# Kernel optimization log

Measured on AMD Instinct MI355X. Metric: run time of the kernel, lower is better.

Reference implementation:

```python
import jax, jax.numpy as jnp
import numpy as np

KERNEL = 3
STRIDE = 1
PADDING = 1


def _extract_patches(x, k, stride, padding, h_out, w_out):
    # x: [B, C, H, W] -> patches [k, k, B, C, h_out, w_out]
    if padding > 0:
        x = jnp.pad(x, ((0, 0), (0, 0), (padding, padding), (padding, padding)))
    rows = []
    for di in range(k):
        cols = []
        for dj in range(k):
            sl = x[:, :, di:di + (h_out - 1) * stride + 1:stride,
                        dj:dj + (w_out - 1) * stride + 1:stride]
            cols.append(sl)
        rows.append(jnp.stack(cols, axis=0))
    return jnp.stack(rows, axis=0)  # [k, k, B, C, h_out, w_out]


def setup_inputs() -> dict:
    key = jax.random.key(0)
    k1, k2 = jax.random.split(key)
    B, C_in, C_out, H, W = 32, 64, 64, 32, 32
    h_out = (H + 2 * PADDING - KERNEL) // STRIDE + 1
    w_out = (W + 2 * PADDING - KERNEL) // STRIDE + 1
    fan_in = C_in * KERNEL ** 2
    x = jax.random.normal(k1, (B, C_in, H, W), dtype=jnp.float32)
    weight = jax.random.normal(
        k2, (h_out, w_out, C_out, C_in, KERNEL, KERNEL), dtype=jnp.float32
    ) / np.sqrt(fan_in).astype(np.float32)
    bias = jnp.zeros((C_out, h_out, w_out), dtype=jnp.float32)
    return {"x": x, "weight": weight, "bias": bias}


def reference(x, weight, bias):
    h_out, w_out = weight.shape[0], weight.shape[1]
    # patches: [k, k, B, C, h_out, w_out]
    patches = _extract_patches(x, KERNEL, STRIDE, PADDING, h_out, w_out)
    # unshared-weight contraction per spatial location
    # weight: [h_out(x), w_out(y), O, C(i), k(k), k(l)]
    out = jnp.einsum('xyoikl,klbixy->boxy', weight, patches)
    return out + bias[None, :, :, :]
```

## Files before the change

kernel.cpp:

```cpp
#include <hip/hip_runtime.h>

#define HH 32
#define WW 32
#define CIN 64
#define COUT 64
#define BATCH 32
#define KTOT 576
#define NPOS 1024
#define KC 16
#define KHALF 288
#define NCW 18
#define WGRP 260

__device__ float g_xT[CIN * 34 * 34 * BATCH];

__global__ __launch_bounds__(256) void repack_kernel(const float* __restrict__ x) {
    __shared__ float tile[32 * 33];
    const int i   = blockIdx.x;
    const int hh  = blockIdx.y;
    const int tid = threadIdx.x;

    float* dst = &g_xT[((i * 34 + hh) * 34) * BATCH];

    if (hh == 0 || hh == 33) {
        for (int idx = tid; idx < 34 * BATCH; idx += 256) dst[idx] = 0.f;
        return;
    }
    const int hs = hh - 1;
#pragma unroll
    for (int bb = 0; bb < 4; ++bb) {
        int b = bb * 8 + (tid >> 5);
        int w = tid & 31;
        tile[b * 33 + w] = x[(b << 16) + (i << 10) + (hs << 5) + w];
    }
    __syncthreads();
#pragma unroll
    for (int q = 0; q < 5; ++q) {
        int ww = q * 8 + (tid >> 5);
        if (ww < 34) {
            int b = tid & 31;
            float v = (ww == 0 || ww == 33) ? 0.f : tile[b * 33 + (ww - 1)];
            dst[ww * BATCH + b] = v;
        }
    }
}

__device__ __forceinline__ void async16(const void* src, void* dst_lds) {
    __builtin_amdgcn_global_load_lds(
        (const __attribute__((address_space(1))) void*)src,
        (__attribute__((address_space(3))) void*)dst_lds,
        16, 0, 0);
}

__global__ __launch_bounds__(128, 2) void local2d_kernel(
    const float* __restrict__ weight,
    const float* __restrict__ bias,
    float* __restrict__ out)
{
    __shared__ float Wl[2][3][4 * WGRP];
    __shared__ float Pl[2][3][KC * BATCH];

    const int wv = threadIdx.x >> 6;
    const int l  = threadIdx.x & 63;

    const int og = l & 7, bg = l >> 3;

    int bid = blockIdx.x;
    int xcd = bid & 7;
    int t   = bid >> 3;
    int y   = ((t >> 5) << 3) | xcd;
    int xw  = t & 31;
    int p   = (y << 5) | xw;

    const int kbase = wv * KHALF;
    const float* wpos  = weight + (long)p * (COUT * KTOT);
    const float* wsrc0 = wpos + (l >> 2) * KTOT + ((l & 3) << 2) + kbase;

    float acc[8][4];
#pragma unroll
    for (int a = 0; a < 8; ++a)
#pragma unroll
        for (int c = 0; c < 4; ++c) acc[a][c] = 0.f;

    auto stage = [&](int c, int bsel) {
        const float* ws = wsrc0 + c * KC;
#pragma unroll
        for (int g = 0; g < 4; ++g)
            async16(ws + g * (16 * KTOT), &Wl[wv][bsel][g * WGRP]);
#pragma unroll
        for (int q = 0; q < 2; ++q) {
            int k  = kbase + c * KC + (q << 3) + (l >> 3);
            int i  = k / 9;
            int r  = k - i * 9;
            int kh = r / 3;
            int kw = r - kh * 3;
            const float* ps =
                &g_xT[(((i * 34) + y + kh) * 34 + xw + kw) * BATCH + ((l & 7) << 2)];
            async16(ps, &Pl[wv][bsel][q * (8 * BATCH)]);
        }
    };

    auto compute = [&](int bsel) {
        const float* Wb = &Wl[wv][bsel][(og >> 1) * WGRP + ((og & 1) << 3) * 16];
        const float* Pb = &Pl[wv][bsel][bg << 2];
#pragma unroll
        for (int kk = 0; kk < KC; kk += 4) {
            float4 pr[4];
#pragma unroll
            for (int j = 0; j < 4; ++j)
                pr[j] = *(const float4*)(Pb + (kk + j) * BATCH);
            const float* prf = (const float*)pr;
#pragma unroll
            for (int oo = 0; oo < 8; ++oo) {
                float4 wr = *(const float4*)(Wb + oo * KC + kk);
#pragma unroll
                for (int bb = 0; bb < 4; ++bb) {
                    float a = acc[oo][bb];
                    a = fmaf(wr.x, prf[0 * 4 + bb], a);
                    a = fmaf(wr.y, prf[1 * 4 + bb], a);
                    a = fmaf(wr.z, prf[2 * 4 + bb], a);
                    a = fmaf(wr.w, prf[3 * 4 + bb], a);
                    acc[oo][bb] = a;
                }
            }
        }
    };

    stage(0, 0);
    stage(1, 1);
    for (int c = 0; c < NCW - 1; ++c) {
        asm volatile("s_waitcnt vmcnt(6)" ::: "memory");
        asm volatile("s_waitcnt lgkmcnt(0)" ::: "memory");
        if (c + 2 < NCW) stage(c + 2, (c + 2) % 3);
        compute(c % 3);
    }
    asm volatile("s_waitcnt vmcnt(0)" ::: "memory");
    compute((NCW - 1) % 3);

    __syncthreads();
    float* R = &Wl[1][0][0];
    if (wv == 1) {
#pragma unroll
        for (int oo = 0; oo < 8; ++oo) {
            int o = (og << 3) + oo;
            *(float4*)(&R[o * 36 + (bg << 2)]) =
                make_float4(acc[oo][0], acc[oo][1], acc[oo][2], acc[oo][3]);
        }
    }
    __syncthreads();
    if (wv == 0) {
#pragma unroll
        for (int oo = 0; oo < 8; ++oo) {
            int o = (og << 3) + oo;
            float bv = bias[(o << 10) + p];
            float4 r = *(const float4*)(&R[o * 36 + (bg << 2)]);
            const float* rf = (const float*)&r;
#pragma unroll
            for (int bb = 0; bb < 4; ++bb) {
                int b = (bg << 2) + bb;
                out[(b << 16) + (o << 10) + p] = acc[oo][bb] + rf[bb] + bv;
            }
        }
    }
}

extern "C" void kernel_launch(void* const* d_in, const int* in_sizes, int n_in,
                              void* d_out, int out_size, void* d_ws, size_t ws_size,
                              hipStream_t stream) {
    const float* x      = (const float*)d_in[0];
    const float* weight = (const float*)d_in[1];
    const float* bias   = (const float*)d_in[2];
    float* out          = (float*)d_out;

    hipLaunchKernelGGL(repack_kernel, dim3(CIN, 34), dim3(256), 0, stream, x);
    hipLaunchKernelGGL(local2d_kernel, dim3(NPOS), dim3(128), 0, stream,
                       weight, bias, out);
}
```

Baseline: 243.1 us.

## Split output channels across two blocks per position with double-buffered LDS staging

Each spatial position is now handled by two blocks, one for each half of the output channels. This doubles the grid and cuts per-thread accumulators from 32 to 16, and launch bounds are raised to allow 4 blocks per SIMD for more occupancy. The weight LDS layout is transposed so that o is contiguous per k, and the pipeline moves from triple to double buffering, issuing the next stage after compute. In exchange, each block loads its patch data twice, since both halves need the full patch.

```diff
diff --git a/kernel.cpp b/kernel.cpp
--- a/kernel.cpp
+++ b/kernel.cpp
@@ -10,7 +10,6 @@
 #define KC 16
 #define KHALF 288
 #define NCW 18
-#define WGRP 260
 
 __device__ float g_xT[CIN * 34 * 34 * BATCH];
 
@@ -52,13 +51,12 @@
         16, 0, 0);
 }
 
-__global__ __launch_bounds__(128, 2) void local2d_kernel(
+__global__ __launch_bounds__(128, 4) void local2d_kernel(
     const float* __restrict__ weight,
     const float* __restrict__ bias,
     float* __restrict__ out)
 {
-    __shared__ float Wl[2][3][4 * WGRP];
-    __shared__ float Pl[2][3][KC * BATCH];
+    __shared__ __align__(16) float lds[4096];
 
     const int wv = threadIdx.x >> 6;
     const int l  = threadIdx.x & 63;
@@ -68,25 +66,33 @@
     int bid = blockIdx.x;
     int xcd = bid & 7;
     int t   = bid >> 3;
-    int y   = ((t >> 5) << 3) | xcd;
-    int xw  = t & 31;
+    int oh  = t & 1;
+    int tt  = t >> 1;
+    int y   = ((tt >> 5) << 3) | xcd;
+    int xw  = tt & 31;
     int p   = (y << 5) | xw;
 
     const int kbase = wv * KHALF;
-    const float* wpos  = weight + (long)p * (COUT * KTOT);
-    const float* wsrc0 = wpos + (l >> 2) * KTOT + ((l & 3) << 2) + kbase;
+    const float* wpos = weight + ((long)p * COUT + (oh << 5)) * KTOT;
 
-    float acc[8][4];
+    const int rem = l & 31;
+    const int wo  = ((rem & 7) << 2) + (rem >> 3);
+    const float* wsrc0 = wpos + wo * KTOT + kbase + ((l >> 5) << 2);
+
+    float* Wb = &lds[wv << 10];
+    float* Pb = &lds[2048 + (wv << 10)];
+
+    float acc[4][4];
 #pragma unroll
-    for (int a = 0; a < 8; ++a)
+    for (int a = 0; a < 4; ++a)
 #pragma unroll
         for (int c = 0; c < 4; ++c) acc[a][c] = 0.f;
 
     auto stage = [&](int c, int bsel) {
         const float* ws = wsrc0 + c * KC;
-#pragma unroll
-        for (int g = 0; g < 4; ++g)
-            async16(ws + g * (16 * KTOT), &Wl[wv][bsel][g * WGRP]);
+        float* wdst = Wb + (bsel << 9);
+        async16(ws,     wdst);
+        async16(ws + 8, wdst + 256);
 #pragma unroll
         for (int q = 0; q < 2; ++q) {
             int k  = kbase + c * KC + (q << 3) + (l >> 3);
@@ -96,23 +102,23 @@
             int kw = r - kh * 3;
             const float* ps =
                 &g_xT[(((i * 34) + y + kh) * 34 + xw + kw) * BATCH + ((l & 7) << 2)];
-            async16(ps, &Pl[wv][bsel][q * (8 * BATCH)]);
+            async16(ps, Pb + (bsel << 9) + (q << 8));
         }
     };
 
     auto compute = [&](int bsel) {
-        const float* Wb = &Wl[wv][bsel][(og >> 1) * WGRP + ((og & 1) << 3) * 16];
-        const float* Pb = &Pl[wv][bsel][bg << 2];
+        const float* Wc = Wb + (bsel << 9);
+        const float* Pc = Pb + (bsel << 9) + (bg << 2);
 #pragma unroll
-        for (int kk = 0; kk < KC; kk += 4) {
+        for (int kkq = 0; kkq < 4; ++kkq) {
             float4 pr[4];
 #pragma unroll
             for (int j = 0; j < 4; ++j)
-                pr[j] = *(const float4*)(Pb + (kk + j) * BATCH);
+                pr[j] = *(const float4*)(Pc + ((kkq << 2) + j) * BATCH);
             const float* prf = (const float*)pr;
 #pragma unroll
-            for (int oo = 0; oo < 8; ++oo) {
-                float4 wr = *(const float4*)(Wb + oo * KC + kk);
+            for (int oo = 0; oo < 4; ++oo) {
+                float4 wr = *(const float4*)(Wc + (kkq << 7) + (oo << 5) + (og << 2));
 #pragma unroll
                 for (int bb = 0; bb < 4; ++bb) {
                     float a = acc[oo][bb];
@@ -128,21 +134,26 @@
 
     stage(0, 0);
     stage(1, 1);
-    for (int c = 0; c < NCW - 1; ++c) {
-        asm volatile("s_waitcnt vmcnt(6)" ::: "memory");
-        asm volatile("s_waitcnt lgkmcnt(0)" ::: "memory");
-        if (c + 2 < NCW) stage(c + 2, (c + 2) % 3);
-        compute(c % 3);
+#pragma unroll 2
+    for (int c = 0; c < NCW; ++c) {
+        if (c < NCW - 1) {
+            asm volatile("s_waitcnt vmcnt(4)" ::: "memory");
+        } else {
+            asm volatile("s_waitcnt vmcnt(0)" ::: "memory");
+        }
+        compute(c & 1);
+        if (c + 2 < NCW) {
+            asm volatile("s_waitcnt lgkmcnt(0)" ::: "memory");
+            stage(c + 2, c & 1);
+        }
     }
-    asm volatile("s_waitcnt vmcnt(0)" ::: "memory");
-    compute((NCW - 1) % 3);
 
     __syncthreads();
-    float* R = &Wl[1][0][0];
+    float* R = &lds[0];
     if (wv == 1) {
 #pragma unroll
-        for (int oo = 0; oo < 8; ++oo) {
-            int o = (og << 3) + oo;
+        for (int oo = 0; oo < 4; ++oo) {
+            int o = (og << 2) + oo;
             *(float4*)(&R[o * 36 + (bg << 2)]) =
                 make_float4(acc[oo][0], acc[oo][1], acc[oo][2], acc[oo][3]);
         }
@@ -150,15 +161,16 @@
     __syncthreads();
     if (wv == 0) {
 #pragma unroll
-        for (int oo = 0; oo < 8; ++oo) {
-            int o = (og << 3) + oo;
-            float bv = bias[(o << 10) + p];
+        for (int oo = 0; oo < 4; ++oo) {
+            int o  = (og << 2) + oo;
+            int of = (oh << 5) + o;
+            float bv = bias[(of << 10) + p];
             float4 r = *(const float4*)(&R[o * 36 + (bg << 2)]);
             const float* rf = (const float*)&r;
 #pragma unroll
             for (int bb = 0; bb < 4; ++bb) {
                 int b = (bg << 2) + bb;
-                out[(b << 16) + (o << 10) + p] = acc[oo][bb] + rf[bb] + bv;
+                out[(b << 16) + (of << 10) + p] = acc[oo][bb] + rf[bb] + bv;
             }
         }
     }
@@ -173,6 +185,6 @@
     float* out          = (float*)d_out;
 
     hipLaunchKernelGGL(repack_kernel, dim3(CIN, 34), dim3(256), 0, stream, x);
-    hipLaunchKernelGGL(local2d_kernel, dim3(NPOS), dim3(128), 0, stream,
+    hipLaunchKernelGGL(local2d_kernel, dim3(2 * NPOS), dim3(128), 0, stream,
                        weight, bias, out);
 }
```

Result: slower. 797.4 us (+228.0%).
